# Kernel tuning notes

Hardware: AMD Instinct MI355X
Metric: run time of the kernel (lower is better)

## Reference

```python
import jax, jax.numpy as jnp
import numpy as np

D_MODEL = 1024
N_HEADS = 16
D_K = D_MODEL // N_HEADS
B, S = 2, 2048


def setup_inputs() -> dict:
    key = jax.random.key(0)
    ks = jax.random.split(key, 12)
    scale = 1.0 / np.sqrt(D_MODEL)
    inp = {
        "query": jax.random.normal(ks[0], (B, S, D_MODEL), jnp.float32),
        "key": jax.random.normal(ks[1], (B, S, D_MODEL), jnp.float32),
        "value": jax.random.normal(ks[2], (B, S, D_MODEL), jnp.float32),
        "mask": jnp.tril(jnp.ones((S, S), dtype=bool))[None, None],  # (1,1,S,S) causal
        "W_q": jax.random.normal(ks[3], (D_MODEL, D_MODEL), jnp.float32) * scale,
        "b_q": jnp.zeros((D_MODEL,), jnp.float32),
        "W_k": jax.random.normal(ks[4], (D_MODEL, D_MODEL), jnp.float32) * scale,
        "b_k": jnp.zeros((D_MODEL,), jnp.float32),
        "W_v": jax.random.normal(ks[5], (D_MODEL, D_MODEL), jnp.float32) * scale,
        "b_v": jnp.zeros((D_MODEL,), jnp.float32),
        "W_o": jax.random.normal(ks[6], (D_MODEL, D_MODEL), jnp.float32) * scale,
        "b_o": jnp.zeros((D_MODEL,), jnp.float32),
    }
    return inp


def reference(query, key, value, mask, W_q, b_q, W_k, b_k, W_v, b_v, W_o, b_o):
    b = query.shape[0]
    # Linear projections (torch Linear: x @ W.T + b), split into heads -> (b,h,s,d_k)
    def proj(x, W, bias):
        y = x @ W.T + bias
        return y.reshape(b, -1, N_HEADS, D_K).transpose(0, 2, 1, 3)

    q = proj(query, W_q, b_q)
    k = proj(key, W_k, b_k)
    v = proj(value, W_v, b_v)

    # scores: (b,h,sq,sk)
    scores = jnp.einsum("bhqd,bhkd->bhqk", q, k) / jnp.sqrt(jnp.float32(D_K)).astype(q.dtype)
    scores = jnp.where(mask, scores, jnp.finfo(scores.dtype).min)
    attn = jax.nn.softmax(scores, axis=-1)
    out = jnp.einsum("bhqk,bhkd->bhqd", attn, v)  # (b,h,sq,d_k)
    out = out.transpose(0, 2, 1, 3).reshape(b, -1, D_MODEL)
    return out @ W_o.T + b_o
```

## Files before the change

kernel.cpp:

```cpp
#include <hip/hip_runtime.h>
#include <hip/hip_bf16.h>
#include <stdint.h>

#define D_MODEL 1024
#define NH 16
#define DK 64
#define BB 2
#define SS 2048
#define MROWS (BB*SS)

typedef __attribute__((ext_vector_type(8))) short bf16x8;
typedef __attribute__((ext_vector_type(4))) float f32x4;

__device__ __forceinline__ short to_bf16(float f) {
  __hip_bfloat16 h = __float2bfloat16(f);
  union { __hip_bfloat16 b; short s; } u; u.b = h; return u.s;
}

__device__ __forceinline__ f32x4 mfma16(bf16x8 a, bf16x8 b, f32x4 c) {
  return __builtin_amdgcn_mfma_f32_16x16x32_bf16(a, b, c, 0, 0, 0);
}

__device__ __forceinline__ void gload_lds16(const void* g, void* l) {
  __builtin_amdgcn_global_load_lds(
      (const __attribute__((address_space(1))) unsigned int*)g,
      (__attribute__((address_space(3))) unsigned int*)l,
      16, 0, 0);
}

__device__ __forceinline__ float max3f(float a, float b, float c) {
  return fmaxf(fmaxf(a, b), c);
}

__global__ __launch_bounds__(256) void cvt7(const float* __restrict__ x0,
                                            const float* __restrict__ x1,
                                            const float* __restrict__ x2,
                                            const float* __restrict__ w0,
                                            const float* __restrict__ w1,
                                            const float* __restrict__ w2,
                                            const float* __restrict__ w3,
                                            short* __restrict__ y0,
                                            short* __restrict__ y1,
                                            short* __restrict__ y2,
                                            short* __restrict__ y3,
                                            short* __restrict__ y4,
                                            short* __restrict__ y5,
                                            short* __restrict__ y6) {
  const int z = blockIdx.z;
  const float* x; short* y; int n;
  switch (z) {
    case 0: x = x0; y = y0; n = MROWS * D_MODEL; break;
    case 1: x = x1; y = y1; n = MROWS * D_MODEL; break;
    case 2: x = x2; y = y2; n = MROWS * D_MODEL; break;
    case 3: x = w0; y = y3; n = D_MODEL * D_MODEL; break;
    case 4: x = w1; y = y4; n = D_MODEL * D_MODEL; break;
    case 5: x = w2; y = y5; n = D_MODEL * D_MODEL; break;
    default: x = w3; y = y6; n = D_MODEL * D_MODEL; break;
  }
  const int i = (blockIdx.x * 256 + threadIdx.x) * 4;
  if (i >= n) return;
  const float4 v = *(const float4*)(x + i);
  short4 o;
  o.x = to_bf16(v.x); o.y = to_bf16(v.y); o.z = to_bf16(v.z); o.w = to_bf16(v.w);
  *(short4*)(y + i) = o;
}

__global__ __launch_bounds__(256) void gemm_qkv(const short* __restrict__ Xq,
                                                const short* __restrict__ Xk,
                                                const short* __restrict__ Xv,
                                                const short* __restrict__ Wq,
                                                const short* __restrict__ Wk,
                                                const short* __restrict__ Wv,
                                                const float* __restrict__ bq,
                                                const float* __restrict__ bk,
                                                const float* __restrict__ bv,
                                                short* __restrict__ Qh,
                                                short* __restrict__ Kh,
                                                short* __restrict__ VT) {
  constexpr int K = 1024, NSTEP = K / 32;
  __shared__ __align__(16) char pool[49152];
  const int z = blockIdx.z;
  const short* A    = z == 0 ? Xq : z == 1 ? Xk : Xv;
  const short* Wt   = z == 0 ? Wq : z == 1 ? Wk : Wv;
  const float* bias = z == 0 ? bq : z == 1 ? bk : bv;

  const int tid = threadIdx.x;
  const int w = tid >> 6, lane = tid & 63;
  const int m0 = blockIdx.x * 128, n0 = blockIdx.y * 128;
  const int wm = w >> 1, wn = w & 1;
  const int fr = lane & 15, fg = lane >> 4;
  const int srow = tid >> 2;
  const int scolS = ((tid & 3) ^ ((srow >> 1) & 3)) * 8;
  const int scolD = (tid & 3) * 8;
  const int fcs = (fg ^ ((fr >> 1) & 3)) * 8;

  f32x4 acc[4][4] = {};

#define QKV_STAGE(buf, k0)                                                    \
  do {                                                                        \
    short* As_ = (short*)(pool + (buf) * 16384);                              \
    short* Bs_ = (short*)(pool + (buf) * 16384 + 8192);                       \
    _Pragma("unroll") for (int i = 0; i < 2; ++i) {                           \
      const int row = i * 64 + srow;                                          \
      gload_lds16(A  + (size_t)(m0 + row) * K + (k0) + scolS,                 \
                  As_ + row * 32 + scolD);                                    \
      gload_lds16(Wt + (size_t)(n0 + row) * K + (k0) + scolS,                 \
                  Bs_ + row * 32 + scolD);                                    \
    }                                                                         \
  } while (0)

  QKV_STAGE(0, 0);
  QKV_STAGE(1, 32);
  asm volatile("s_waitcnt vmcnt(4)" ::: "memory");
  __syncthreads();

  for (int t = 0; t < NSTEP; ++t) {
    if (t + 2 < NSTEP) QKV_STAGE((t + 2) % 3, (t + 2) * 32);

    const short* Ab = (const short*)(pool + (t % 3) * 16384);
    const short* Bb = (const short*)(pool + (t % 3) * 16384 + 8192);
    bf16x8 af[4], bfr[4];
#pragma unroll
    for (int i = 0; i < 4; ++i) {
      af[i]  = *(const bf16x8*)(Ab + (wm * 64 + i * 16 + fr) * 32 + fcs);
      bfr[i] = *(const bf16x8*)(Bb + (wn * 64 + i * 16 + fr) * 32 + fcs);
    }
    __builtin_amdgcn_s_setprio(1);
#pragma unroll
    for (int mi = 0; mi < 4; ++mi)
#pragma unroll
      for (int ni = 0; ni < 4; ++ni)
        acc[mi][ni] = mfma16(af[mi], bfr[ni], acc[mi][ni]);
    __builtin_amdgcn_s_setprio(0);

    if (t + 2 < NSTEP)
      asm volatile("s_waitcnt vmcnt(4)" ::: "memory");
    else
      asm volatile("s_waitcnt vmcnt(0)" ::: "memory");
    __syncthreads();
  }
#undef QKV_STAGE

  if (z < 2) {
    const float scale = (z == 0) ? 0.18033688011112042f : 1.0f;
    short* dst = (z == 0) ? Qh : Kh;
#pragma unroll
    for (int mi = 0; mi < 4; ++mi)
#pragma unroll
      for (int ni = 0; ni < 4; ++ni) {
        const int col = n0 + wn * 64 + ni * 16 + fr;
        const float bval = bias[col];
        const int h = col >> 6, d = col & 63;
#pragma unroll
        for (int r = 0; r < 4; ++r) {
          const int row = m0 + wm * 64 + mi * 16 + fg * 4 + r;
          const float val = (acc[mi][ni][r] + bval) * scale;
          const int b = row >> 11, s = row & (SS - 1);
          dst[((size_t)(b * NH + h) * SS + s) * DK + d] = to_bf16(val);
        }
      }
  } else {
    short* trs = (short*)pool;
#pragma unroll
    for (int mi = 0; mi < 4; ++mi)
#pragma unroll
      for (int ni = 0; ni < 4; ++ni) {
        const int dl = wn * 64 + ni * 16 + fr;
        const int s0 = wm * 64 + mi * 16 + fg * 4;
        const float bval = bias[n0 + dl];
        short4 sv = {to_bf16(acc[mi][ni][0] + bval), to_bf16(acc[mi][ni][1] + bval),
                     to_bf16(acc[mi][ni][2] + bval), to_bf16(acc[mi][ni][3] + bval)};
        *(short4*)(trs + dl * 128 + (s0 ^ ((dl & 7) << 3))) = sv;
      }
    __syncthreads();
    const int b = m0 >> 11, sbase = m0 & (SS - 1);
#pragma unroll
    for (int rep = 0; rep < 8; ++rep) {
      const int dl = (tid >> 4) + rep * 16;
      const int s0 = (tid & 15) * 8;
      const bf16x8 vv = *(const bf16x8*)(trs + dl * 128 + (s0 ^ ((dl & 7) << 3)));
      const int col = n0 + dl;
      const int h = col >> 6, d = col & 63;
      *(bf16x8*)(VT + ((size_t)(b * NH + h) * DK + d) * SS + sbase + s0) = vv;
    }
  }
}

__global__ __launch_bounds__(256) void gemm_out(const short* __restrict__ A,
                                                const short* __restrict__ Wt,
                                                const float* __restrict__ bias,
                                                float* __restrict__ Y) {
  constexpr int K = 1024, NSTEP = K / 32;
  __shared__ __align__(16) char pool[36864];
  const int tid = threadIdx.x;
  const int w = tid >> 6, lane = tid & 63;
  const int m0 = blockIdx.x * 128, n0 = blockIdx.y * 64;
  const int wm = w >> 1, wn = w & 1;
  const int fr = lane & 15, fg = lane >> 4;
  const int srow = tid >> 2;
  const int scolS = ((tid & 3) ^ ((srow >> 1) & 3)) * 8;
  const int scolD = (tid & 3) * 8;
  const int fcs = (fg ^ ((fr >> 1) & 3)) * 8;

  f32x4 acc[4][2] = {};

#define OUT_STAGE(buf, k0)                                                    \
  do {                                                                        \
    short* As_ = (short*)(pool + (buf) * 12288);                              \
    short* Bs_ = (short*)(pool + (buf) * 12288 + 8192);                       \
    _Pragma("unroll") for (int i = 0; i < 2; ++i) {                           \
      const int row = i * 64 + srow;                                          \
      gload_lds16(A + (size_t)(m0 + row) * K + (k0) + scolS,                  \
                  As_ + row * 32 + scolD);                                    \
    }                                                                         \
    gload_lds16(Wt + (size_t)(n0 + srow) * K + (k0) + scolS,                  \
                Bs_ + srow * 32 + scolD);                                     \
  } while (0)

  OUT_STAGE(0, 0);
  OUT_STAGE(1, 32);
  asm volatile("s_waitcnt vmcnt(3)" ::: "memory");
  __syncthreads();

  for (int t = 0; t < NSTEP; ++t) {
    if (t + 2 < NSTEP) OUT_STAGE((t + 2) % 3, (t + 2) * 32);

    const short* Ab = (const short*)(pool + (t % 3) * 12288);
    const short* Bb = (const short*)(pool + (t % 3) * 12288 + 8192);
    bf16x8 af[4], bfr[2];
#pragma unroll
    for (int i = 0; i < 4; ++i)
      af[i] = *(const bf16x8*)(Ab + (wm * 64 + i * 16 + fr) * 32 + fcs);
#pragma unroll
    for (int i = 0; i < 2; ++i)
      bfr[i] = *(const bf16x8*)(Bb + (wn * 32 + i * 16 + fr) * 32 + fcs);
    __builtin_amdgcn_s_setprio(1);
#pragma unroll
    for (int mi = 0; mi < 4; ++mi)
#pragma unroll
      for (int ni = 0; ni < 2; ++ni)
        acc[mi][ni] = mfma16(af[mi], bfr[ni], acc[mi][ni]);
    __builtin_amdgcn_s_setprio(0);

    if (t + 2 < NSTEP)
      asm volatile("s_waitcnt vmcnt(3)" ::: "memory");
    else
      asm volatile("s_waitcnt vmcnt(0)" ::: "memory");
    __syncthreads();
  }
#undef OUT_STAGE

#pragma unroll
  for (int mi = 0; mi < 4; ++mi)
#pragma unroll
    for (int ni = 0; ni < 2; ++ni) {
      const int col = n0 + wn * 32 + ni * 16 + fr;
      const float bval = bias[col];
#pragma unroll
      for (int r = 0; r < 4; ++r) {
        const int row = m0 + wm * 64 + mi * 16 + fg * 4 + r;
        Y[(size_t)row * D_MODEL + col] = acc[mi][ni][r] + bval;
      }
    }
}

__global__ __launch_bounds__(256) void attn_kernel(const short* __restrict__ Qh,
                                                   const short* __restrict__ Kh,
                                                   const short* __restrict__ VT,
                                                   short* __restrict__ AO) {
  __shared__ short Ks[2][64 * 64];
  __shared__ short Vs[2][64 * 64];
  __shared__ short P_lds[4][16 * 64];

  const int tid = threadIdx.x, w = tid >> 6, lane = tid & 63;
  const int fr = lane & 15, fg = lane >> 4;
  const int kr = fg * 4;
  const int swz = (fr & 7) << 4;

  const int bid = blockIdx.x;
  const int lid = ((bid & 7) << 7) | (bid >> 3);
  const int bh = lid >> 5;
  const int i5 = lid & 31;
  const int j = (i5 & 1) ? (i5 >> 1) : (31 - (i5 >> 1));
  const int b = bh >> 4, h = bh & 15;
  const int qb = j * 64;
  const int T = j + 1;

  const short* Qp = Qh + (size_t)bh * SS * DK;
  const short* Kp = Kh + (size_t)bh * SS * DK;
  const short* Vp = VT + (size_t)bh * DK * SS;

  const int sc_c = tid & 7;
  const int sc_r = tid >> 3;

  bf16x8 qf[2];
#pragma unroll
  for (int hh = 0; hh < 2; ++hh)
    qf[hh] = *(const bf16x8*)(Qp + (size_t)(qb + w * 16 + fr) * DK + hh * 32 + fg * 8);

  const short onev = (fr == 0) ? (short)0x3F80 : (short)0;
  const bf16x8 af4 = {onev, onev, onev, onev, onev, onev, onev, onev};

  f32x4 o[5] = {};
  float m_run = -1e30f;
  f32x4 stA[4], stB[4];

#define STAGE_K(buf, kk0)                                                     \
  do {                                                                        \
    _Pragma("unroll") for (int p = 0; p < 2; ++p) {                           \
      const int row = p * 32 + sc_r;                                          \
      const int sc = sc_c ^ (row & 7);                                        \
      gload_lds16(Kp + (size_t)((kk0) + row) * DK + sc * 8,                   \
                  &Ks[buf][row * 64 + sc_c * 8]);                             \
    }                                                                         \
  } while (0)
#define STAGE_V(buf, kk0)                                                     \
  do {                                                                        \
    _Pragma("unroll") for (int p = 0; p < 2; ++p) {                           \
      const int row = p * 32 + sc_r;                                          \
      const int sc = sc_c ^ (row & 7);                                        \
      gload_lds16(Vp + (size_t)row * SS + (kk0) + sc * 8,                     \
                  &Vs[buf][row * 64 + sc_c * 8]);                             \
    }                                                                         \
  } while (0)

#define SOFTMAX_PV(ST, bufPrev)                                               \
  do {                                                                        \
    float mm0 = fmaxf(fmaxf(ST[0][0], ST[0][1]), fmaxf(ST[0][2], ST[0][3]));  \
    float mm1 = fmaxf(fmaxf(ST[1][0], ST[1][1]), fmaxf(ST[1][2], ST[1][3]));  \
    float mm2 = fmaxf(fmaxf(ST[2][0], ST[2][1]), fmaxf(ST[2][2], ST[2][3]));  \
    float mm3 = fmaxf(fmaxf(ST[3][0], ST[3][1]), fmaxf(ST[3][2], ST[3][3]));  \
    float pmax = fmaxf(fmaxf(mm0, mm1), fmaxf(mm2, mm3));                     \
    pmax = fmaxf(pmax, __shfl_xor(pmax, 16));                                 \
    pmax = fmaxf(pmax, __shfl_xor(pmax, 32));                                 \
    if (!__all(pmax <= m_run + 11.0f)) {                                      \
      const float mn = fmaxf(m_run, pmax);                                    \
      const float al = __builtin_amdgcn_exp2f(m_run - mn);                    \
      m_run = mn;                                                             \
      _Pragma("unroll") for (int t = 0; t < 5; ++t)                           \
        _Pragma("unroll") for (int r = 0; r < 4; ++r) o[t][r] *= al;          \
    }                                                                         \
    {                                                                         \
      char* base = (char*)P_lds[w];                                           \
      _Pragma("unroll") for (int kt = 0; kt < 4; ++kt) {                      \
        short4 sv;                                                            \
        sv.x = to_bf16(__builtin_amdgcn_exp2f(ST[kt][0] - m_run));            \
        sv.y = to_bf16(__builtin_amdgcn_exp2f(ST[kt][1] - m_run));            \
        sv.z = to_bf16(__builtin_amdgcn_exp2f(ST[kt][2] - m_run));            \
        sv.w = to_bf16(__builtin_amdgcn_exp2f(ST[kt][3] - m_run));            \
        *(short4*)(base + ((fr * 128 + kt * 32 + fg * 8) ^ swz)) = sv;        \
      }                                                                       \
    }                                                                         \
    asm volatile("s_waitcnt lgkmcnt(0)" ::: "memory");                        \
    {                                                                         \
      const char* VsB = (const char*)Vs[bufPrev];                             \
      __builtin_amdgcn_s_setprio(1);                                          \
      _Pragma("unroll") for (int c = 0; c < 2; ++c) {                         \
        const bf16x8 pf = *(const bf16x8*)((const char*)P_lds[w] +            \
                                           ((fr * 128 + c * 64 + fg * 16) ^ swz)); \
        _Pragma("unroll") for (int t = 0; t < 4; ++t) {                       \
          const bf16x8 vfb = *(const bf16x8*)(VsB + (t * 16 + fr) * 128 +     \
                                              ((c * 64 + fg * 16) ^ swz));    \
          o[t] = mfma16(vfb, pf, o[t]);                                       \
        }                                                                     \
        o[4] = mfma16(af4, pf, o[4]);                                         \
      }                                                                       \
      __builtin_amdgcn_s_setprio(0);                                          \
    }                                                                         \
  } while (0)

#define STEP(CUR, PREV, g)                                                    \
  do {                                                                        \
    if ((g) + 1 < T) STAGE_K(((g) + 1) & 1, ((g) + 1) * 64);                  \
    {                                                                         \
      const char* KsB = (const char*)Ks[(g) & 1];                             \
      __builtin_amdgcn_s_setprio(1);                                          \
      _Pragma("unroll") for (int kt = 0; kt < 4; ++kt) {                      \
        const bf16x8 k0f = *(const bf16x8*)(KsB + (kt * 16 + fr) * 128 + ((fg * 16) ^ swz)); \
        const bf16x8 k1f = *(const bf16x8*)(KsB + (kt * 16 + fr) * 128 + ((64 + fg * 16) ^ swz)); \
        f32x4 zz = {};                                                        \
        zz = mfma16(k0f, qf[0], zz);                                          \
        zz = mfma16(k1f, qf[1], zz);                                          \
        CUR[kt] = zz;                                                         \
      }                                                                       \
      __builtin_amdgcn_s_setprio(0);                                          \
    }                                                                         \
    if ((g) == T - 1) {                                                       \
      _Pragma("unroll") for (int kt = 0; kt < 4; ++kt)                        \
        _Pragma("unroll") for (int r = 0; r < 4; ++r)                         \
          if (kt * 16 + kr + r > w * 16 + fr) CUR[kt][r] = -1e30f;            \
    }                                                                         \
    if ((g) > 0) SOFTMAX_PV(PREV, ((g) - 1) & 1);                             \
    __syncthreads();                                                          \
    if ((g) + 1 < T) {                                                        \
      STAGE_V(((g) + 1) & 1, ((g) + 1) * 64);                                 \
      asm volatile("s_waitcnt vmcnt(2)" ::: "memory");                        \
    } else {                                                                  \
      asm volatile("s_waitcnt vmcnt(0)" ::: "memory");                        \
    }                                                                         \
  } while (0)

  STAGE_K(0, 0);
  STAGE_V(0, 0);
  asm volatile("s_waitcnt vmcnt(2)" ::: "memory");
  __syncthreads();

  for (int gg = 0; gg < T; gg += 2) {
    STEP(stA, stB, gg);
    if (gg + 1 < T) STEP(stB, stA, gg + 1);
  }

  if (T & 1) SOFTMAX_PV(stA, (T - 1) & 1);
  else       SOFTMAX_PV(stB, (T - 1) & 1);

  const float l = __shfl(o[4][0], fr);
  const float inv = 1.0f / l;
  const int s = qb + w * 16 + fr;
#pragma unroll
  for (int t = 0; t < 4; ++t) {
    short4 ov = {to_bf16(o[t][0] * inv), to_bf16(o[t][1] * inv),
                 to_bf16(o[t][2] * inv), to_bf16(o[t][3] * inv)};
    *(short4*)(AO + (size_t)(b * SS + s) * D_MODEL + h * 64 + t * 16 + kr) = ov;
  }
#undef STEP
#undef SOFTMAX_PV
#undef STAGE_K
#undef STAGE_V
}

extern "C" void kernel_launch(void* const* d_in, const int* in_sizes, int n_in,
                              void* d_out, int out_size, void* d_ws, size_t ws_size,
                              hipStream_t stream) {
  const float* q  = (const float*)d_in[0];
  const float* k  = (const float*)d_in[1];
  const float* v  = (const float*)d_in[2];
  const float* Wq = (const float*)d_in[4];
  const float* bq = (const float*)d_in[5];
  const float* Wk = (const float*)d_in[6];
  const float* bk = (const float*)d_in[7];
  const float* Wv = (const float*)d_in[8];
  const float* bv = (const float*)d_in[9];
  const float* Wo = (const float*)d_in[10];
  const float* bo = (const float*)d_in[11];

  char* ws = (char*)d_ws;
  const size_t MB = 1u << 20;
  short* Xq = (short*)(ws + 0 * MB);
  short* Xk = (short*)(ws + 8 * MB);
  short* Xv = (short*)(ws + 16 * MB);
  short* Bq = (short*)(ws + 24 * MB);
  short* Bk = (short*)(ws + 26 * MB);
  short* Bv = (short*)(ws + 28 * MB);
  short* Bo = (short*)(ws + 30 * MB);
  short* Qh = (short*)(ws + 32 * MB);
  short* Kh = (short*)(ws + 40 * MB);
  short* VT = (short*)(ws + 48 * MB);
  short* AO = (short*)(ws + 56 * MB);

  cvt7<<<dim3(MROWS * D_MODEL / 1024, 1, 7), 256, 0, stream>>>(
      q, k, v, Wq, Wk, Wv, Wo, Xq, Xk, Xv, Bq, Bk, Bv, Bo);

  gemm_qkv<<<dim3(MROWS / 128, D_MODEL / 128, 3), 256, 0, stream>>>(
      Xq, Xk, Xv, Bq, Bk, Bv, bq, bk, bv, Qh, Kh, VT);

  attn_kernel<<<dim3(1024), 256, 0, stream>>>(Qh, Kh, VT, AO);

  gemm_out<<<dim3(MROWS / 128, D_MODEL / 64), 256, 0, stream>>>(AO, Bo, bo, (float*)d_out);
}
```

Baseline: 137.9 us.

## Pair causal query tiles per attention block and use 128-key steps; narrow QKV GEMM tiles

The attention kernel now gives each block two query tiles, j and 31-j, so every block does the same 17 key steps under the causal mask. Each step covers 128 keys split into two 64-key halves, and the partial output is stored and reset when processing switches to the second tile. The grid is halved to 512 blocks, and more registers and LDS per block may lower occupancy. The QKV projection GEMM switches to 128x64 tiles, doubling its block count to improve CU fill.

```diff
diff --git a/kernel.cpp b/kernel.cpp
--- a/kernel.cpp
+++ b/kernel.cpp
@@ -78,7 +78,7 @@
                                                 short* __restrict__ Kh,
                                                 short* __restrict__ VT) {
   constexpr int K = 1024, NSTEP = K / 32;
-  __shared__ __align__(16) char pool[49152];
+  __shared__ __align__(16) char pool[36864];
   const int z = blockIdx.z;
   const short* A    = z == 0 ? Xq : z == 1 ? Xk : Xv;
   const short* Wt   = z == 0 ? Wq : z == 1 ? Wk : Wv;
@@ -86,7 +86,7 @@
 
   const int tid = threadIdx.x;
   const int w = tid >> 6, lane = tid & 63;
-  const int m0 = blockIdx.x * 128, n0 = blockIdx.y * 128;
+  const int m0 = blockIdx.x * 128, n0 = blockIdx.y * 64;
   const int wm = w >> 1, wn = w & 1;
   const int fr = lane & 15, fg = lane >> 4;
   const int srow = tid >> 2;
@@ -94,47 +94,48 @@
   const int scolD = (tid & 3) * 8;
   const int fcs = (fg ^ ((fr >> 1) & 3)) * 8;
 
-  f32x4 acc[4][4] = {};
+  f32x4 acc[4][2] = {};
 
 #define QKV_STAGE(buf, k0)                                                    \
   do {                                                                        \
-    short* As_ = (short*)(pool + (buf) * 16384);                              \
-    short* Bs_ = (short*)(pool + (buf) * 16384 + 8192);                       \
+    short* As_ = (short*)(pool + (buf) * 12288);                              \
+    short* Bs_ = (short*)(pool + (buf) * 12288 + 8192);                       \
     _Pragma("unroll") for (int i = 0; i < 2; ++i) {                           \
       const int row = i * 64 + srow;                                          \
-      gload_lds16(A  + (size_t)(m0 + row) * K + (k0) + scolS,                 \
+      gload_lds16(A + (size_t)(m0 + row) * K + (k0) + scolS,                  \
                   As_ + row * 32 + scolD);                                    \
-      gload_lds16(Wt + (size_t)(n0 + row) * K + (k0) + scolS,                 \
-                  Bs_ + row * 32 + scolD);                                    \
-    }                                                                         \
+    }                                                                         \
+    gload_lds16(Wt + (size_t)(n0 + srow) * K + (k0) + scolS,                  \
+                Bs_ + srow * 32 + scolD);                                     \
   } while (0)
 
   QKV_STAGE(0, 0);
   QKV_STAGE(1, 32);
-  asm volatile("s_waitcnt vmcnt(4)" ::: "memory");
+  asm volatile("s_waitcnt vmcnt(3)" ::: "memory");
   __syncthreads();
 
   for (int t = 0; t < NSTEP; ++t) {
     if (t + 2 < NSTEP) QKV_STAGE((t + 2) % 3, (t + 2) * 32);
 
-    const short* Ab = (const short*)(pool + (t % 3) * 16384);
-    const short* Bb = (const short*)(pool + (t % 3) * 16384 + 8192);
-    bf16x8 af[4], bfr[4];
-#pragma unroll
-    for (int i = 0; i < 4; ++i) {
-      af[i]  = *(const bf16x8*)(Ab + (wm * 64 + i * 16 + fr) * 32 + fcs);
-      bfr[i] = *(const bf16x8*)(Bb + (wn * 64 + i * 16 + fr) * 32 + fcs);
-    }
+    const short* Ab = (const short*)(pool + (t % 3) * 12288);
+    const short* Bb = (const short*)(pool + (t % 3) * 12288 + 8192);
+    bf16x8 af[4], bfr[2];
+#pragma unroll
+    for (int i = 0; i < 4; ++i)
+      af[i] = *(const bf16x8*)(Ab + (wm * 64 + i * 16 + fr) * 32 + fcs);
+#pragma unroll
+    for (int i = 0; i < 2; ++i)
+      bfr[i] = *(const bf16x8*)(Bb + (wn * 32 + i * 16 + fr) * 32 + fcs);
     __builtin_amdgcn_s_setprio(1);
 #pragma unroll
     for (int mi = 0; mi < 4; ++mi)
 #pragma unroll
-      for (int ni = 0; ni < 4; ++ni)
+      for (int ni = 0; ni < 2; ++ni)
         acc[mi][ni] = mfma16(af[mi], bfr[ni], acc[mi][ni]);
     __builtin_amdgcn_s_setprio(0);
 
     if (t + 2 < NSTEP)
-      asm volatile("s_waitcnt vmcnt(4)" ::: "memory");
+      asm volatile("s_waitcnt vmcnt(3)" ::: "memory");
     else
       asm volatile("s_waitcnt vmcnt(0)" ::: "memory");
     __syncthreads();
@@ -147,8 +148,8 @@
 #pragma unroll
     for (int mi = 0; mi < 4; ++mi)
 #pragma unroll
-      for (int ni = 0; ni < 4; ++ni) {
-        const int col = n0 + wn * 64 + ni * 16 + fr;
+      for (int ni = 0; ni < 2; ++ni) {
+        const int col = n0 + wn * 32 + ni * 16 + fr;
         const float bval = bias[col];
         const int h = col >> 6, d = col & 63;
 #pragma unroll
@@ -164,8 +165,8 @@
 #pragma unroll
     for (int mi = 0; mi < 4; ++mi)
 #pragma unroll
-      for (int ni = 0; ni < 4; ++ni) {
-        const int dl = wn * 64 + ni * 16 + fr;
+      for (int ni = 0; ni < 2; ++ni) {
+        const int dl = wn * 32 + ni * 16 + fr;
         const int s0 = wm * 64 + mi * 16 + fg * 4;
         const float bval = bias[n0 + dl];
         short4 sv = {to_bf16(acc[mi][ni][0] + bval), to_bf16(acc[mi][ni][1] + bval),
@@ -175,7 +176,7 @@
     __syncthreads();
     const int b = m0 >> 11, sbase = m0 & (SS - 1);
 #pragma unroll
-    for (int rep = 0; rep < 8; ++rep) {
+    for (int rep = 0; rep < 4; ++rep) {
       const int dl = (tid >> 4) + rep * 16;
       const int s0 = (tid & 15) * 8;
       const bf16x8 vv = *(const bf16x8*)(trs + dl * 128 + (s0 ^ ((dl & 7) << 3)));
@@ -268,8 +269,8 @@
                                                    const short* __restrict__ Kh,
                                                    const short* __restrict__ VT,
                                                    short* __restrict__ AO) {
-  __shared__ short Ks[2][64 * 64];
-  __shared__ short Vs[2][64 * 64];
+  __shared__ short Ks[2][2][64 * 64];
+  __shared__ short Vs[2][2][64 * 64];
   __shared__ short P_lds[4][16 * 64];
 
   const int tid = threadIdx.x, w = tid >> 6, lane = tid & 63;
@@ -278,13 +279,10 @@
   const int swz = (fr & 7) << 4;
 
   const int bid = blockIdx.x;
-  const int lid = ((bid & 7) << 7) | (bid >> 3);
-  const int bh = lid >> 5;
-  const int i5 = lid & 31;
-  const int j = (i5 & 1) ? (i5 >> 1) : (31 - (i5 >> 1));
+  const int lid = ((bid & 7) << 6) | (bid >> 3);
+  const int bh = lid >> 4;
+  const int j = lid & 15;
   const int b = bh >> 4, h = bh & 15;
-  const int qb = j * 64;
-  const int T = j + 1;
 
   const short* Qp = Qh + (size_t)bh * SS * DK;
   const short* Kp = Kh + (size_t)bh * SS * DK;
@@ -293,44 +291,51 @@
   const int sc_c = tid & 7;
   const int sc_r = tid >> 3;
 
+  const int T0 = (j + 2) >> 1;
+  const int koff0 = j * 64 - (T0 - 1) * 128;
+  const int koff1 = (31 - j) * 64 - (16 - T0) * 128;
+
   bf16x8 qf[2];
 #pragma unroll
   for (int hh = 0; hh < 2; ++hh)
-    qf[hh] = *(const bf16x8*)(Qp + (size_t)(qb + w * 16 + fr) * DK + hh * 32 + fg * 8);
+    qf[hh] = *(const bf16x8*)(Qp + (size_t)(j * 64 + w * 16 + fr) * DK + hh * 32 + fg * 8);
 
   const short onev = (fr == 0) ? (short)0x3F80 : (short)0;
   const bf16x8 af4 = {onev, onev, onev, onev, onev, onev, onev, onev};
 
   f32x4 o[5] = {};
   float m_run = -1e30f;
-  f32x4 stA[4], stB[4];
-
+  f32x4 stA[8], stB[8];
+
+#define KK0(g) ((((g) < T0) ? (g) : ((g) - T0)) * 128)
 #define STAGE_K(buf, kk0)                                                     \
   do {                                                                        \
+    _Pragma("unroll") for (int hf = 0; hf < 2; ++hf)                          \
     _Pragma("unroll") for (int p = 0; p < 2; ++p) {                           \
       const int row = p * 32 + sc_r;                                          \
       const int sc = sc_c ^ (row & 7);                                        \
-      gload_lds16(Kp + (size_t)((kk0) + row) * DK + sc * 8,                   \
-                  &Ks[buf][row * 64 + sc_c * 8]);                             \
+      gload_lds16(Kp + (size_t)((kk0) + hf * 64 + row) * DK + sc * 8,         \
+                  &Ks[buf][hf][row * 64 + sc_c * 8]);                         \
     }                                                                         \
   } while (0)
 #define STAGE_V(buf, kk0)                                                     \
   do {                                                                        \
+    _Pragma("unroll") for (int hf = 0; hf < 2; ++hf)                          \
     _Pragma("unroll") for (int p = 0; p < 2; ++p) {                           \
       const int row = p * 32 + sc_r;                                          \
       const int sc = sc_c ^ (row & 7);                                        \
-      gload_lds16(Vp + (size_t)row * SS + (kk0) + sc * 8,                     \
-                  &Vs[buf][row * 64 + sc_c * 8]);                             \
+      gload_lds16(Vp + (size_t)row * SS + (kk0) + hf * 64 + sc * 8,           \
+                  &Vs[buf][hf][row * 64 + sc_c * 8]);                         \
     }                                                                         \
   } while (0)
 
 #define SOFTMAX_PV(ST, bufPrev)                                               \
   do {                                                                        \
-    float mm0 = fmaxf(fmaxf(ST[0][0], ST[0][1]), fmaxf(ST[0][2], ST[0][3]));  \
-    float mm1 = fmaxf(fmaxf(ST[1][0], ST[1][1]), fmaxf(ST[1][2], ST[1][3]));  \
-    float mm2 = fmaxf(fmaxf(ST[2][0], ST[2][1]), fmaxf(ST[2][2], ST[2][3]));  \
-    float mm3 = fmaxf(fmaxf(ST[3][0], ST[3][1]), fmaxf(ST[3][2], ST[3][3]));  \
-    float pmax = fmaxf(fmaxf(mm0, mm1), fmaxf(mm2, mm3));                     \
+    float mm[8];                                                              \
+    _Pragma("unroll") for (int i = 0; i < 8; ++i)                             \
+      mm[i] = fmaxf(fmaxf(ST[i][0], ST[i][1]), fmaxf(ST[i][2], ST[i][3]));    \
+    float pmax = fmaxf(max3f(mm[0], mm[1], mm[2]),                            \
+                       fmaxf(max3f(mm[3], mm[4], mm[5]), fmaxf(mm[6], mm[7]))); \
     pmax = fmaxf(pmax, __shfl_xor(pmax, 16));                                 \
     pmax = fmaxf(pmax, __shfl_xor(pmax, 32));                                 \
     if (!__all(pmax <= m_run + 11.0f)) {                                      \
@@ -340,20 +345,18 @@
       _Pragma("unroll") for (int t = 0; t < 5; ++t)                           \
         _Pragma("unroll") for (int r = 0; r < 4; ++r) o[t][r] *= al;          \
     }                                                                         \
-    {                                                                         \
+    _Pragma("unroll") for (int hf = 0; hf < 2; ++hf) {                        \
       char* base = (char*)P_lds[w];                                           \
       _Pragma("unroll") for (int kt = 0; kt < 4; ++kt) {                      \
         short4 sv;                                                            \
-        sv.x = to_bf16(__builtin_amdgcn_exp2f(ST[kt][0] - m_run));            \
-        sv.y = to_bf16(__builtin_amdgcn_exp2f(ST[kt][1] - m_run));            \
-        sv.z = to_bf16(__builtin_amdgcn_exp2f(ST[kt][2] - m_run));            \
-        sv.w = to_bf16(__builtin_amdgcn_exp2f(ST[kt][3] - m_run));            \
+        sv.x = to_bf16(__builtin_amdgcn_exp2f(ST[hf * 4 + kt][0] - m_run));   \
+        sv.y = to_bf16(__builtin_amdgcn_exp2f(ST[hf * 4 + kt][1] - m_run));   \
+        sv.z = to_bf16(__builtin_amdgcn_exp2f(ST[hf * 4 + kt][2] - m_run));   \
+        sv.w = to_bf16(__builtin_amdgcn_exp2f(ST[hf * 4 + kt][3] - m_run));   \
         *(short4*)(base + ((fr * 128 + kt * 32 + fg * 8) ^ swz)) = sv;        \
       }                                                                       \
-    }                                                                         \
-    asm volatile("s_waitcnt lgkmcnt(0)" ::: "memory");                        \
-    {                                                                         \
-      const char* VsB = (const char*)Vs[bufPrev];                             \
+      asm volatile("s_waitcnt lgkmcnt(0)" ::: "memory");                      \
+      const char* VsB = (const char*)Vs[bufPrev][hf];                         \
       __builtin_amdgcn_s_setprio(1);                                          \
       _Pragma("unroll") for (int c = 0; c < 2; ++c) {                         \
         const bf16x8 pf = *(const bf16x8*)((const char*)P_lds[w] +            \
@@ -371,61 +374,82 @@
 
 #define STEP(CUR, PREV, g)                                                    \
   do {                                                                        \
-    if ((g) + 1 < T) STAGE_K(((g) + 1) & 1, ((g) + 1) * 64);                  \
+    if ((g) == T0) {                                                          \
+      _Pragma("unroll") for (int hh = 0; hh < 2; ++hh)                        \
+        qf[hh] = *(const bf16x8*)(Qp + (size_t)((31 - j) * 64 + w * 16 + fr) * DK + hh * 32 + fg * 8); \
+    }                                                                         \
+    if ((g) + 1 < 17) STAGE_K(((g) + 1) & 1, KK0((g) + 1));                   \
     {                                                                         \
-      const char* KsB = (const char*)Ks[(g) & 1];                             \
       __builtin_amdgcn_s_setprio(1);                                          \
-      _Pragma("unroll") for (int kt = 0; kt < 4; ++kt) {                      \
-        const bf16x8 k0f = *(const bf16x8*)(KsB + (kt * 16 + fr) * 128 + ((fg * 16) ^ swz)); \
-        const bf16x8 k1f = *(const bf16x8*)(KsB + (kt * 16 + fr) * 128 + ((64 + fg * 16) ^ swz)); \
-        f32x4 zz = {};                                                        \
-        zz = mfma16(k0f, qf[0], zz);                                          \
-        zz = mfma16(k1f, qf[1], zz);                                          \
-        CUR[kt] = zz;                                                         \
+      _Pragma("unroll") for (int hf = 0; hf < 2; ++hf) {                      \
+        const char* KsB = (const char*)Ks[(g) & 1][hf];                       \
+        _Pragma("unroll") for (int kt = 0; kt < 4; ++kt) {                    \
+          const bf16x8 k0f = *(const bf16x8*)(KsB + (kt * 16 + fr) * 128 + ((fg * 16) ^ swz)); \
+          const bf16x8 k1f = *(const bf16x8*)(KsB + (kt * 16 + fr) * 128 + ((64 + fg * 16) ^ swz)); \
+          f32x4 zz = {};                                                      \
+          zz = mfma16(k0f, qf[0], zz);                                        \
+          zz = mfma16(k1f, qf[1], zz);                                        \
+          CUR[hf * 4 + kt] = zz;                                              \
+        }                                                                     \
       }                                                                       \
       __builtin_amdgcn_s_setprio(0);                                          \
     }                                                                         \
-    if ((g) == T - 1) {                                                       \
-      _Pragma("unroll") for (int kt = 0; kt < 4; ++kt)                        \
-        _Pragma("unroll") for (int r = 0; r < 4; ++r)                         \
-          if (kt * 16 + kr + r > w * 16 + fr) CUR[kt][r] = -1e30f;            \
-    }                                                                         \
-    if ((g) > 0) SOFTMAX_PV(PREV, ((g) - 1) & 1);                             \
+    if ((g) == T0 - 1 || (g) == 16) {                                         \
+      const int koff = ((g) == 16) ? koff1 : koff0;                           \
+      _Pragma("unroll") for (int hf = 0; hf < 2; ++hf)                        \
+        _Pragma("unroll") for (int kt = 0; kt < 4; ++kt)                      \
+          _Pragma("unroll") for (int r = 0; r < 4; ++r)                       \
+            if (hf * 64 + kt * 16 + kr + r > koff + w * 16 + fr)              \
+              CUR[hf * 4 + kt][r] = -1e30f;                                   \
+    }                                                                         \
+    if ((g) > 0) {                                                            \
+      SOFTMAX_PV(PREV, ((g) - 1) & 1);                                        \
+      if ((g) == T0) {                                                        \
+        store_o(j * 64);                                                      \
+        _Pragma("unroll") for (int t = 0; t < 5; ++t)                         \
+          _Pragma("unroll") for (int r = 0; r < 4; ++r) o[t][r] = 0.f;        \
+        m_run = -1e30f;                                                       \
+      }                                                                       \
+    }                                                                         \
     __syncthreads();                                                          \
-    if ((g) + 1 < T) {                                                        \
-      STAGE_V(((g) + 1) & 1, ((g) + 1) * 64);                                 \
-      asm volatile("s_waitcnt vmcnt(2)" ::: "memory");                        \
+    if ((g) + 1 < 17) {                                                       \
+      STAGE_V(((g) + 1) & 1, KK0((g) + 1));                                   \
+      asm volatile("s_waitcnt vmcnt(4)" ::: "memory");                        \
     } else {                                                                  \
       asm volatile("s_waitcnt vmcnt(0)" ::: "memory");                        \
     }                                                                         \
   } while (0)
 
+  auto store_o = [&](int qbase) {
+    const float l = __shfl(o[4][0], fr);
+    const float inv = 1.0f / l;
+    const int s = qbase + w * 16 + fr;
+#pragma unroll
+    for (int t = 0; t < 4; ++t) {
+      short4 ov = {to_bf16(o[t][0] * inv), to_bf16(o[t][1] * inv),
+                   to_bf16(o[t][2] * inv), to_bf16(o[t][3] * inv)};
+      *(short4*)(AO + (size_t)(b * SS + s) * D_MODEL + h * 64 + t * 16 + kr) = ov;
+    }
+  };
+
   STAGE_K(0, 0);
   STAGE_V(0, 0);
-  asm volatile("s_waitcnt vmcnt(2)" ::: "memory");
+  asm volatile("s_waitcnt vmcnt(0)" ::: "memory");
   __syncthreads();
 
-  for (int gg = 0; gg < T; gg += 2) {
+  for (int gg = 0; gg < 16; gg += 2) {
     STEP(stA, stB, gg);
-    if (gg + 1 < T) STEP(stB, stA, gg + 1);
+    STEP(stB, stA, gg + 1);
   }
-
-  if (T & 1) SOFTMAX_PV(stA, (T - 1) & 1);
-  else       SOFTMAX_PV(stB, (T - 1) & 1);
-
-  const float l = __shfl(o[4][0], fr);
-  const float inv = 1.0f / l;
-  const int s = qb + w * 16 + fr;
-#pragma unroll
-  for (int t = 0; t < 4; ++t) {
-    short4 ov = {to_bf16(o[t][0] * inv), to_bf16(o[t][1] * inv),
-                 to_bf16(o[t][2] * inv), to_bf16(o[t][3] * inv)};
-    *(short4*)(AO + (size_t)(b * SS + s) * D_MODEL + h * 64 + t * 16 + kr) = ov;
-  }
+  STEP(stA, stB, 16);
+
+  SOFTMAX_PV(stA, 0);
+  store_o((31 - j) * 64);
 #undef STEP
 #undef SOFTMAX_PV
 #undef STAGE_K
 #undef STAGE_V
+#undef KK0
 }
 
 extern "C" void kernel_launch(void* const* d_in, const int* in_sizes, int n_in,
@@ -460,10 +484,10 @@
   cvt7<<<dim3(MROWS * D_MODEL / 1024, 1, 7), 256, 0, stream>>>(
       q, k, v, Wq, Wk, Wv, Wo, Xq, Xk, Xv, Bq, Bk, Bv, Bo);
 
-  gemm_qkv<<<dim3(MROWS / 128, D_MODEL / 128, 3), 256, 0, stream>>>(
+  gemm_qkv<<<dim3(MROWS / 128, D_MODEL / 64, 3), 256, 0, stream>>>(
       Xq, Xk, Xv, Bq, Bk, Bv, bq, bk, bv, Qh, Kh, VT);
 
-  attn_kernel<<<dim3(1024), 256, 0, stream>>>(Qh, Kh, VT, AO);
+  attn_kernel<<<dim3(512), 256, 0, stream>>>(Qh, Kh, VT, AO);
 
   gemm_out<<<dim3(MROWS / 128, D_MODEL / 64), 256, 0, stream>>>(AO, Bo, bo, (float*)d_out);
 }
```

New measurement: 117.7 us. 14.7% less time.
